# Optimization experiments

Measured on AMD Instinct MI355X. Metric: run time of the kernel, lower is better.

## Reference

```python
import jax, jax.numpy as jnp
import numpy as np

N = 50000      # nodes
E = 800000     # edges (avg degree 16)
G = 128        # graphs in batch
IN = 128       # in_channels
H = 128        # hidden_dim
C = 10         # num_classes


def setup_inputs() -> dict:
    key = jax.random.key(0)
    ks = jax.random.split(key, 8)
    x = jax.random.normal(ks[0], (N, IN), dtype=jnp.float32)
    edge_index = jax.random.randint(ks[1], (2, E), 0, N)
    edge_attr = jax.random.uniform(ks[2], (E,), dtype=jnp.float32)
    batch = jnp.sort(jax.random.randint(ks[3], (N,), 0, G))
    def glorot(k, fan_in, fan_out):
        return jax.random.normal(k, (fan_in, fan_out), dtype=jnp.float32) / np.float32(np.sqrt(fan_in))
    return {
        "x": x,
        "edge_index": edge_index,
        "edge_attr": edge_attr,
        "batch": batch,
        "W1": glorot(ks[4], IN, H), "b1": jnp.zeros((H,), jnp.float32),
        "W2": glorot(ks[5], H, H), "b2": jnp.zeros((H,), jnp.float32),
        "W3": glorot(ks[6], H, C), "b3": jnp.zeros((C,), jnp.float32),
    }


def gcn_conv(x, src, dst, ew, W, b, n):
    # symmetric GCN normalization (self-loops already appended, weight 1)
    deg = jax.ops.segment_sum(ew, dst, num_segments=n)            # [N]
    dinv = jnp.where(deg > 0, jax.lax.rsqrt(deg), 0.0)
    norm = dinv[src] * ew * dinv[dst]                             # [E+N]
    h = x @ W                                                     # [N, out]
    agg = jax.ops.segment_sum(h[src] * norm[:, None], dst, num_segments=n)
    return agg + b


def reference(x, edge_index, edge_attr, batch, W1, b1, W2, b2, W3, b3):
    n = x.shape[0]
    loop = jnp.arange(n)
    src = jnp.concatenate([edge_index[0], loop])
    dst = jnp.concatenate([edge_index[1], loop])
    ew = jnp.concatenate([edge_attr, jnp.ones((n,), edge_attr.dtype)])
    h = jax.nn.relu(gcn_conv(x, src, dst, ew, W1, b1, n))   # dropout is identity in eval
    h = jax.nn.relu(gcn_conv(h, src, dst, ew, W2, b2, n))
    h = gcn_conv(h, src, dst, ew, W3, b3, n)                 # [N, C]
    # global mean pool over graphs
    sums = jax.ops.segment_sum(h, batch, num_segments=G)     # [G, C]
    cnt = jax.ops.segment_sum(jnp.ones((n,), h.dtype), batch, num_segments=G)
    pooled = sums / jnp.maximum(cnt, 1.0)[:, None]
    return jax.nn.log_softmax(pooled, axis=1)
```

## Files before the change

### kernel.cpp

```cpp
#include <hip/hip_runtime.h>

#define NN 50000
#define NE 800000
#define NG 128
#define DIM 128
#define CO 10
#define CAP 64
#define NPB 2048
#define GEMB 782

typedef unsigned short ushort;
typedef unsigned int uint;
typedef __attribute__((ext_vector_type(8))) short short8;
typedef __attribute__((ext_vector_type(4))) float floatx4;

static __device__ __forceinline__ ushort f2bf(float f) {
    uint u = __float_as_uint(f);
    uint r = (u + 0x7FFF + ((u >> 16) & 1)) >> 16;
    return (ushort)r;
}
#define EWS (1.0f / 65535.0f)

__global__ void k_prep(const float* __restrict__ W1, const float* __restrict__ W2,
                       ushort* __restrict__ wt1, ushort* __restrict__ wt2,
                       int* __restrict__ cnt) {
    int i = blockIdx.x * 256 + threadIdx.x;
    if (i < 16384) {
        wt1[(i & 127) * 128 + (i >> 7)] = f2bf(W1[i]);
    } else if (i < 32768) {
        int j = i - 16384;
        wt2[(j & 127) * 128 + (j >> 7)] = f2bf(W2[j]);
    } else if (i < 32768 + NN) {
        cnt[i - 32768] = 0;
    }
}

__global__ void k_ell(const int* __restrict__ src, const int* __restrict__ dst,
                      const float* __restrict__ ew, int* __restrict__ cnt,
                      uint* __restrict__ ell) {
    int e = blockIdx.x * blockDim.x + threadIdx.x;
    if (e >= NE) return;
    int d = dst[e], s = src[e];
    int slot = atomicAdd(&cnt[d], 1);
    if (slot < CAP) {
        uint w16 = (uint)__float2uint_rn(ew[e] * 65535.0f);
        ell[(size_t)d * CAP + slot] = (w16 << 16) | (uint)s;
    }
}

static __device__ __forceinline__ void gemm_tile(const void* Ain, int abf,
                                                 const ushort* Wt,
                                                 const float* dglob, const float* dlds,
                                                 ushort* C, int M, int r0, int lane) {
    int quad = lane >> 4;
    int mcol = lane & 15;
    int arow = r0 + mcol;
    if (arow >= M) arow = M - 1;
    floatx4 acc[8];
#pragma unroll
    for (int t = 0; t < 8; t++) acc[t] = (floatx4){0.0f, 0.0f, 0.0f, 0.0f};
    const ushort* Ab = (const ushort*)Ain;
    const float*  Af = (const float*)Ain;
#pragma unroll
    for (int kk = 0; kk < 4; kk++) {
        int koff = kk * 32 + quad * 8;
        short8 a;
        if (abf) {
            a = *(const short8*)&Ab[(size_t)arow * 128 + koff];
        } else {
            const float* ap = &Af[(size_t)arow * 128 + koff];
            float4 x0 = *(const float4*)ap;
            float4 x1 = *(const float4*)(ap + 4);
            union { short8 v; ushort u[8]; } ua;
            ua.u[0] = f2bf(x0.x); ua.u[1] = f2bf(x0.y); ua.u[2] = f2bf(x0.z); ua.u[3] = f2bf(x0.w);
            ua.u[4] = f2bf(x1.x); ua.u[5] = f2bf(x1.y); ua.u[6] = f2bf(x1.z); ua.u[7] = f2bf(x1.w);
            a = ua.v;
        }
#pragma unroll
        for (int t = 0; t < 8; t++) {
            short8 b = *(const short8*)&Wt[(size_t)(t * 16 + mcol) * 128 + koff];
            acc[t] = __builtin_amdgcn_mfma_f32_16x16x32_bf16(a, b, acc[t], 0, 0, 0);
        }
    }
#pragma unroll
    for (int reg = 0; reg < 4; reg++) {
        int row = r0 + quad * 4 + reg;
        if (row < M) {
            float di = dglob ? dglob[row] : (dlds ? dlds[quad * 4 + reg] : 1.0f);
            ushort* cp = &C[(size_t)row * 128];
#pragma unroll
            for (int t = 0; t < 8; t++) cp[t * 16 + mcol] = f2bf(di * acc[t][reg]);
        }
    }
}

__global__ __launch_bounds__(256) void k_gemm1(const float* __restrict__ x,
                                               const ushort* __restrict__ wt1,
                                               const int* __restrict__ cnt,
                                               const uint* __restrict__ ell,
                                               float* __restrict__ dinv,
                                               ushort* __restrict__ hb) {
    __shared__ float sdinv[4][16];
    int wv = threadIdx.x >> 6;
    int lane = threadIdx.x & 63;
    int r0 = blockIdx.x * 64 + wv * 16;
#pragma unroll 4
    for (int r = 0; r < 16; r++) {
        int row = r0 + r;
        if (row < NN) {
            int n = cnt[row];
            float w = (lane < n) ? (float)(ell[(size_t)row * CAP + lane] >> 16) * EWS : 0.0f;
#pragma unroll
            for (int off = 32; off; off >>= 1) w += __shfl_down(w, off);
            if (lane == 0) {
                float dv = rsqrtf(1.0f + w);
                dinv[row] = dv;
                sdinv[wv][r] = dv;
            }
        }
    }
    gemm_tile(x, 0, wt1, nullptr, &sdinv[wv][0], hb, NN, r0, lane);
}

__global__ __launch_bounds__(256) void k_gemm2(const ushort* __restrict__ A,
                                               const ushort* __restrict__ wt2,
                                               const float* __restrict__ dinv,
                                               ushort* __restrict__ C) {
    int wv = threadIdx.x >> 6;
    int lane = threadIdx.x & 63;
    gemm_tile(A, 1, wt2, dinv, nullptr, C, NN, blockIdx.x * 64 + wv * 16, lane);
}

__global__ __launch_bounds__(256) void k_gather1(const int* __restrict__ cnt,
                                                 const uint* __restrict__ ell,
                                                 const float* __restrict__ dinv,
                                                 const ushort* __restrict__ h,
                                                 const float* __restrict__ b,
                                                 ushort* __restrict__ outp) {
    int node = blockIdx.x * 4 + (threadIdx.x >> 6);
    int lane = threadIdx.x & 63;
    if (node >= NN) return;
    int n = cnt[node];
    float di = dinv[node];
    uint rec = ell[(size_t)node * CAP + lane];
    int ce = (int)(rec & 0xffffu);
    float we = (float)(rec >> 16) * EWS;
    uint hp = *(const uint*)&h[(size_t)node * 128 + lane * 2];
    float ax = __uint_as_float(hp << 16);
    float ay = __uint_as_float(hp & 0xffff0000u);
    int j = 0;
    for (; j + 3 < n; j += 4) {
        int s0 = __shfl(ce, j + 0), s1 = __shfl(ce, j + 1);
        int s2 = __shfl(ce, j + 2), s3 = __shfl(ce, j + 3);
        float w0 = __shfl(we, j + 0), w1 = __shfl(we, j + 1);
        float w2 = __shfl(we, j + 2), w3 = __shfl(we, j + 3);
        uint p0 = *(const uint*)&h[(size_t)s0 * 128 + lane * 2];
        uint p1 = *(const uint*)&h[(size_t)s1 * 128 + lane * 2];
        uint p2 = *(const uint*)&h[(size_t)s2 * 128 + lane * 2];
        uint p3 = *(const uint*)&h[(size_t)s3 * 128 + lane * 2];
        ax += w0 * __uint_as_float(p0 << 16) + w1 * __uint_as_float(p1 << 16)
            + w2 * __uint_as_float(p2 << 16) + w3 * __uint_as_float(p3 << 16);
        ay += w0 * __uint_as_float(p0 & 0xffff0000u) + w1 * __uint_as_float(p1 & 0xffff0000u)
            + w2 * __uint_as_float(p2 & 0xffff0000u) + w3 * __uint_as_float(p3 & 0xffff0000u);
    }
    for (; j < n; j++) {
        int s0 = __shfl(ce, j);
        float w0 = __shfl(we, j);
        uint p0 = *(const uint*)&h[(size_t)s0 * 128 + lane * 2];
        ax += w0 * __uint_as_float(p0 << 16);
        ay += w0 * __uint_as_float(p0 & 0xffff0000u);
    }
    ax = fmaxf(di * ax + b[lane * 2 + 0], 0.0f);
    ay = fmaxf(di * ay + b[lane * 2 + 1], 0.0f);
    uint o = ((uint)f2bf(ay) << 16) | (uint)f2bf(ax);
    *(uint*)&outp[(size_t)node * 128 + lane * 2] = o;
}

__global__ __launch_bounds__(256) void k_gather2z(const int* __restrict__ cnt,
                                                  const uint* __restrict__ ell,
                                                  const float* __restrict__ dinv,
                                                  const ushort* __restrict__ h,
                                                  const float* __restrict__ b,
                                                  const float* __restrict__ W3,
                                                  float* __restrict__ z) {
    int lane = threadIdx.x & 63;
    int gwave = blockIdx.x * 4 + (threadIdx.x >> 6);
    float w3a[10], w3b[10];
    const float* wrow = &W3[lane * 20];
#pragma unroll
    for (int f = 0; f < 10; f++) { w3a[f] = wrow[f]; w3b[f] = wrow[10 + f]; }
    float bx = b[lane * 2 + 0], by = b[lane * 2 + 1];

    for (int node = gwave; node < NN; node += 12500) {
        int n = cnt[node];
        float di = dinv[node];
        uint rec = ell[(size_t)node * CAP + lane];
        int ce = (int)(rec & 0xffffu);
        float we = (float)(rec >> 16) * EWS;
        uint hp = *(const uint*)&h[(size_t)node * 128 + lane * 2];
        float ax = __uint_as_float(hp << 16);
        float ay = __uint_as_float(hp & 0xffff0000u);
        int j = 0;
        for (; j + 3 < n; j += 4) {
            int s0 = __shfl(ce, j + 0), s1 = __shfl(ce, j + 1);
            int s2 = __shfl(ce, j + 2), s3 = __shfl(ce, j + 3);
            float w0 = __shfl(we, j + 0), w1 = __shfl(we, j + 1);
            float w2 = __shfl(we, j + 2), w3 = __shfl(we, j + 3);
            uint p0 = *(const uint*)&h[(size_t)s0 * 128 + lane * 2];
            uint p1 = *(const uint*)&h[(size_t)s1 * 128 + lane * 2];
            uint p2 = *(const uint*)&h[(size_t)s2 * 128 + lane * 2];
            uint p3 = *(const uint*)&h[(size_t)s3 * 128 + lane * 2];
            ax += w0 * __uint_as_float(p0 << 16) + w1 * __uint_as_float(p1 << 16)
                + w2 * __uint_as_float(p2 << 16) + w3 * __uint_as_float(p3 << 16);
            ay += w0 * __uint_as_float(p0 & 0xffff0000u) + w1 * __uint_as_float(p1 & 0xffff0000u)
                + w2 * __uint_as_float(p2 & 0xffff0000u) + w3 * __uint_as_float(p3 & 0xffff0000u);
        }
        for (; j < n; j++) {
            int s0 = __shfl(ce, j);
            float w0 = __shfl(we, j);
            uint p0 = *(const uint*)&h[(size_t)s0 * 128 + lane * 2];
            ax += w0 * __uint_as_float(p0 << 16);
            ay += w0 * __uint_as_float(p0 & 0xffff0000u);
        }
        ax = fmaxf(di * ax + bx, 0.0f);
        ay = fmaxf(di * ay + by, 0.0f);
        float p[10];
#pragma unroll
        for (int f = 0; f < 10; f++) p[f] = ax * w3a[f] + ay * w3b[f];
#pragma unroll
        for (int off = 32; off; off >>= 1) {
#pragma unroll
            for (int f = 0; f < 10; f++) p[f] += __shfl_down(p[f], off);
        }
        if (lane == 0) {
            float* zp = &z[(size_t)node * 10];
#pragma unroll
            for (int f = 0; f < 10; f++) zp[f] = di * p[f];
        }
    }
}

__global__ __launch_bounds__(256) void k_pool_node(const int* __restrict__ cnt,
                                                   const uint* __restrict__ ell,
                                                   const float* __restrict__ dinv,
                                                   const float* __restrict__ z,
                                                   const int* __restrict__ batch,
                                                   float* __restrict__ partial) {
    __shared__ float ls[NG * CO + NG];
    for (int i = threadIdx.x; i < NG * CO + NG; i += 256) ls[i] = 0.0f;
    __syncthreads();
    int lane = threadIdx.x & 63;
    int gwave = blockIdx.x * 4 + (threadIdx.x >> 6);
    for (int node = gwave; node < NN; node += NPB * 4) {
        int n = cnt[node];
        float w = 0.0f; int s = 0;
        if (lane < n) {
            uint rec = ell[(size_t)node * CAP + lane];
            s = (int)(rec & 0xffffu);
            w = (float)(rec >> 16) * EWS;
        } else if (lane == n) {
            s = node;
            w = 1.0f;
        }
        const float* zp = &z[(size_t)s * 10];
        float v[10];
#pragma unroll
        for (int f = 0; f < 10; f++) v[f] = w * zp[f];
#pragma unroll
        for (int off = 32; off; off >>= 1) {
#pragma unroll
            for (int f = 0; f < 10; f++) v[f] += __shfl_down(v[f], off);
        }
        if (lane == 0) {
            int g = batch[node];
            float di = dinv[node];
            float* lp = &ls[g * 10];
#pragma unroll
            for (int f = 0; f < 10; f++) atomicAdd(&lp[f], di * v[f]);
            atomicAdd(&ls[NG * CO + g], 1.0f);
        }
    }
    __syncthreads();
    float* pb = &partial[(size_t)blockIdx.x * (NG * CO + NG)];
    for (int i = threadIdx.x; i < NG * CO + NG; i += 256) pb[i] = ls[i];
}

__global__ __launch_bounds__(256) void k_pool_final(const float* __restrict__ partial,
                                                    const float* __restrict__ b3,
                                                    float* __restrict__ out) {
    __shared__ float red[4][11];
    int g = blockIdx.x;
    int t = threadIdx.x;
    int lane = t & 63, wv = t >> 6;
    float v[10]; float c = 0.0f;
#pragma unroll
    for (int f = 0; f < 10; f++) v[f] = 0.0f;
    for (int b = t; b < NPB; b += 256) {
        const float* pb = &partial[(size_t)b * (NG * CO + NG)];
#pragma unroll
        for (int f = 0; f < 10; f++) v[f] += pb[g * 10 + f];
        c += pb[NG * CO + g];
    }
#pragma unroll
    for (int off = 32; off; off >>= 1) {
#pragma unroll
        for (int f = 0; f < 10; f++) v[f] += __shfl_down(v[f], off);
        c += __shfl_down(c, off);
    }
    if (lane == 0) {
#pragma unroll
        for (int f = 0; f < 10; f++) red[wv][f] = v[f];
        red[wv][10] = c;
    }
    __syncthreads();
    if (t == 0) {
        float p[10], m = -1e30f;
        float cc = red[0][10] + red[1][10] + red[2][10] + red[3][10];
        cc = fmaxf(cc, 1.0f);
#pragma unroll
        for (int f = 0; f < 10; f++) {
            p[f] = (red[0][f] + red[1][f] + red[2][f] + red[3][f]) / cc + b3[f];
            m = fmaxf(m, p[f]);
        }
        float ssum = 0.0f;
#pragma unroll
        for (int f = 0; f < 10; f++) ssum += __expf(p[f] - m);
        float lse = m + __logf(ssum);
#pragma unroll
        for (int f = 0; f < 10; f++) out[g * 10 + f] = p[f] - lse;
    }
}

extern "C" void kernel_launch(void* const* d_in, const int* in_sizes, int n_in,
                              void* d_out, int out_size, void* d_ws, size_t ws_size,
                              hipStream_t stream) {
    const float* x     = (const float*)d_in[0];
    const int*   ei    = (const int*)d_in[1];
    const float* ea    = (const float*)d_in[2];
    const int*   batch = (const int*)d_in[3];
    const float* W1    = (const float*)d_in[4];
    const float* b1    = (const float*)d_in[5];
    const float* W2    = (const float*)d_in[6];
    const float* b2    = (const float*)d_in[7];
    const float* W3    = (const float*)d_in[8];
    const float* b3    = (const float*)d_in[9];
    float* out = (float*)d_out;
    float* ws  = (float*)d_ws;

    const int* esrc = ei;
    const int* edst = ei + NE;

    ushort* hb      = (ushort*)ws;
    ushort* gb      = (ushort*)(ws + 3200000);
    float*  z       = ws + 6400000;
    float*  dinv    = ws + 6900000;
    int*    cnt     = (int*)(ws + 6950000);
    uint*   ell     = (uint*)(ws + 7000000);
    ushort* wt1     = (ushort*)(ws + 10200000);
    ushort* wt2     = (ushort*)(ws + 10210000);
    float*  partial = (float*)hb;

    k_prep<<<330, 256, 0, stream>>>(W1, W2, wt1, wt2, cnt);
    k_ell<<<(NE + 255) / 256, 256, 0, stream>>>(esrc, edst, ea, cnt, ell);
    k_gemm1<<<GEMB, 256, 0, stream>>>(x, wt1, cnt, ell, dinv, hb);
    k_gather1<<<(NN + 3) / 4, 256, 0, stream>>>(cnt, ell, dinv, hb, b1, gb);
    k_gemm2<<<GEMB, 256, 0, stream>>>(gb, wt2, dinv, hb);
    k_gather2z<<<3125, 256, 0, stream>>>(cnt, ell, dinv, hb, b2, W3, z);
    k_pool_node<<<NPB, 256, 0, stream>>>(cnt, ell, dinv, z, batch, partial);
    k_pool_final<<<NG, 256, 0, stream>>>(partial, b3, out);
}
```

Baseline: 325.0 us.

## Replace per-node atomic counters with sentinel-filled ELL rows and CAS slot insertion

Removes the per-destination counter array. Each edge is inserted with atomicCAS probing from a hashed slot into an ELL row pre-filled with a sentinel. Readers find the valid entries with a wave ballot and compact them with ds_permute, which gives both the count and the packed records. This avoids contended atomicAdd on counters, but it has to initialise the whole 50000x64 ELL array (12.8 MB) in the prep kernel and adds ballot/permute work to every gather.

```diff
diff --git a/kernel.cpp b/kernel.cpp
--- a/kernel.cpp
+++ b/kernel.cpp
@@ -8,7 +8,9 @@
 #define CAP 64
 #define NPB 2048
 #define GEMB 782
-
+#define SENT 0xFFFFFFFFu
+
+typedef unsigned long long ull;
 typedef unsigned short ushort;
 typedef unsigned int uint;
 typedef __attribute__((ext_vector_type(8))) short short8;
@@ -21,30 +23,55 @@
 }
 #define EWS (1.0f / 65535.0f)
 
+static __device__ __forceinline__ int row_load(const uint* __restrict__ ell,
+                                               int node, int lane,
+                                               int* ce, float* we) {
+    uint rec = ell[(size_t)node * CAP + lane];
+    bool valid = (rec != SENT);
+    ull mask = __ballot(valid);
+    int n = __popcll(mask);
+    ull below = (lane == 63) ? mask & ~(1ull << 63) : mask & ((1ull << lane) - 1ull);
+    int pos;
+    if (valid) {
+        pos = __popcll(below);
+    } else {
+        ull ibelow = ~mask & ((lane == 63) ? ~(1ull << 63) : ((1ull << lane) - 1ull));
+        pos = n + __popcll(ibelow);
+    }
+    uint crec = (uint)__builtin_amdgcn_ds_permute(pos << 2, (int)rec);
+    *ce = (int)(crec & 0xffffu);
+    *we = (float)(crec >> 16) * EWS;
+    return n;
+}
+
 __global__ void k_prep(const float* __restrict__ W1, const float* __restrict__ W2,
                        ushort* __restrict__ wt1, ushort* __restrict__ wt2,
-                       int* __restrict__ cnt) {
+                       uint* __restrict__ ell) {
     int i = blockIdx.x * 256 + threadIdx.x;
     if (i < 16384) {
         wt1[(i & 127) * 128 + (i >> 7)] = f2bf(W1[i]);
     } else if (i < 32768) {
         int j = i - 16384;
         wt2[(j & 127) * 128 + (j >> 7)] = f2bf(W2[j]);
-    } else if (i < 32768 + NN) {
-        cnt[i - 32768] = 0;
+    } else if (i < 32768 + NN * CAP) {
+        ell[i - 32768] = SENT;
     }
 }
 
 __global__ void k_ell(const int* __restrict__ src, const int* __restrict__ dst,
-                      const float* __restrict__ ew, int* __restrict__ cnt,
-                      uint* __restrict__ ell) {
+                      const float* __restrict__ ew, uint* __restrict__ ell) {
     int e = blockIdx.x * blockDim.x + threadIdx.x;
     if (e >= NE) return;
     int d = dst[e], s = src[e];
-    int slot = atomicAdd(&cnt[d], 1);
-    if (slot < CAP) {
-        uint w16 = (uint)__float2uint_rn(ew[e] * 65535.0f);
-        ell[(size_t)d * CAP + slot] = (w16 << 16) | (uint)s;
+    uint w16 = (uint)__float2uint_rn(ew[e] * 65535.0f);
+    uint rec = (w16 << 16) | (uint)s;
+    uint* row = &ell[(size_t)d * CAP];
+    uint h0 = (uint)e & 63u;
+#pragma unroll 1
+    for (int p = 0; p < CAP; p++) {
+        uint slot = (h0 + p) & 63u;
+        uint old = atomicCAS(&row[slot], SENT, rec);
+        if (old == SENT) break;
     }
 }
 
@@ -96,7 +123,6 @@
 
 __global__ __launch_bounds__(256) void k_gemm1(const float* __restrict__ x,
                                                const ushort* __restrict__ wt1,
-                                               const int* __restrict__ cnt,
                                                const uint* __restrict__ ell,
                                                float* __restrict__ dinv,
                                                ushort* __restrict__ hb) {
@@ -108,8 +134,8 @@
     for (int r = 0; r < 16; r++) {
         int row = r0 + r;
         if (row < NN) {
-            int n = cnt[row];
-            float w = (lane < n) ? (float)(ell[(size_t)row * CAP + lane] >> 16) * EWS : 0.0f;
+            uint rec = ell[(size_t)row * CAP + lane];
+            float w = (rec != SENT) ? (float)(rec >> 16) * EWS : 0.0f;
 #pragma unroll
             for (int off = 32; off; off >>= 1) w += __shfl_down(w, off);
             if (lane == 0) {
@@ -131,8 +157,7 @@
     gemm_tile(A, 1, wt2, dinv, nullptr, C, NN, blockIdx.x * 64 + wv * 16, lane);
 }
 
-__global__ __launch_bounds__(256) void k_gather1(const int* __restrict__ cnt,
-                                                 const uint* __restrict__ ell,
+__global__ __launch_bounds__(256) void k_gather1(const uint* __restrict__ ell,
                                                  const float* __restrict__ dinv,
                                                  const ushort* __restrict__ h,
                                                  const float* __restrict__ b,
@@ -140,11 +165,9 @@
     int node = blockIdx.x * 4 + (threadIdx.x >> 6);
     int lane = threadIdx.x & 63;
     if (node >= NN) return;
-    int n = cnt[node];
+    int ce; float we;
+    int n = row_load(ell, node, lane, &ce, &we);
     float di = dinv[node];
-    uint rec = ell[(size_t)node * CAP + lane];
-    int ce = (int)(rec & 0xffffu);
-    float we = (float)(rec >> 16) * EWS;
     uint hp = *(const uint*)&h[(size_t)node * 128 + lane * 2];
     float ax = __uint_as_float(hp << 16);
     float ay = __uint_as_float(hp & 0xffff0000u);
@@ -176,8 +199,7 @@
     *(uint*)&outp[(size_t)node * 128 + lane * 2] = o;
 }
 
-__global__ __launch_bounds__(256) void k_gather2z(const int* __restrict__ cnt,
-                                                  const uint* __restrict__ ell,
+__global__ __launch_bounds__(256) void k_gather2z(const uint* __restrict__ ell,
                                                   const float* __restrict__ dinv,
                                                   const ushort* __restrict__ h,
                                                   const float* __restrict__ b,
@@ -192,11 +214,9 @@
     float bx = b[lane * 2 + 0], by = b[lane * 2 + 1];
 
     for (int node = gwave; node < NN; node += 12500) {
-        int n = cnt[node];
+        int ce; float we;
+        int n = row_load(ell, node, lane, &ce, &we);
         float di = dinv[node];
-        uint rec = ell[(size_t)node * CAP + lane];
-        int ce = (int)(rec & 0xffffu);
-        float we = (float)(rec >> 16) * EWS;
         uint hp = *(const uint*)&h[(size_t)node * 128 + lane * 2];
         float ax = __uint_as_float(hp << 16);
         float ay = __uint_as_float(hp & 0xffff0000u);
@@ -240,8 +260,7 @@
     }
 }
 
-__global__ __launch_bounds__(256) void k_pool_node(const int* __restrict__ cnt,
-                                                   const uint* __restrict__ ell,
+__global__ __launch_bounds__(256) void k_pool_node(const uint* __restrict__ ell,
                                                    const float* __restrict__ dinv,
                                                    const float* __restrict__ z,
                                                    const int* __restrict__ batch,
@@ -252,12 +271,12 @@
     int lane = threadIdx.x & 63;
     int gwave = blockIdx.x * 4 + (threadIdx.x >> 6);
     for (int node = gwave; node < NN; node += NPB * 4) {
-        int n = cnt[node];
+        int ce; float we;
+        int n = row_load(ell, node, lane, &ce, &we);
         float w = 0.0f; int s = 0;
         if (lane < n) {
-            uint rec = ell[(size_t)node * CAP + lane];
-            s = (int)(rec & 0xffffu);
-            w = (float)(rec >> 16) * EWS;
+            s = ce;
+            w = we;
         } else if (lane == n) {
             s = node;
             w = 1.0f;
@@ -354,18 +373,17 @@
     ushort* gb      = (ushort*)(ws + 3200000);
     float*  z       = ws + 6400000;
     float*  dinv    = ws + 6900000;
-    int*    cnt     = (int*)(ws + 6950000);
     uint*   ell     = (uint*)(ws + 7000000);
     ushort* wt1     = (ushort*)(ws + 10200000);
     ushort* wt2     = (ushort*)(ws + 10210000);
     float*  partial = (float*)hb;
 
-    k_prep<<<330, 256, 0, stream>>>(W1, W2, wt1, wt2, cnt);
-    k_ell<<<(NE + 255) / 256, 256, 0, stream>>>(esrc, edst, ea, cnt, ell);
-    k_gemm1<<<GEMB, 256, 0, stream>>>(x, wt1, cnt, ell, dinv, hb);
-    k_gather1<<<(NN + 3) / 4, 256, 0, stream>>>(cnt, ell, dinv, hb, b1, gb);
+    k_prep<<<(32768 + NN * CAP + 255) / 256, 256, 0, stream>>>(W1, W2, wt1, wt2, ell);
+    k_ell<<<(NE + 255) / 256, 256, 0, stream>>>(esrc, edst, ea, ell);
+    k_gemm1<<<GEMB, 256, 0, stream>>>(x, wt1, ell, dinv, hb);
+    k_gather1<<<(NN + 3) / 4, 256, 0, stream>>>(ell, dinv, hb, b1, gb);
     k_gemm2<<<GEMB, 256, 0, stream>>>(gb, wt2, dinv, hb);
-    k_gather2z<<<3125, 256, 0, stream>>>(cnt, ell, dinv, hb, b2, W3, z);
-    k_pool_node<<<NPB, 256, 0, stream>>>(cnt, ell, dinv, z, batch, partial);
+    k_gather2z<<<3125, 256, 0, stream>>>(ell, dinv, hb, b2, W3, z);
+    k_pool_node<<<NPB, 256, 0, stream>>>(ell, dinv, z, batch, partial);
     k_pool_final<<<NG, 256, 0, stream>>>(partial, b3, out);
 }
```

Measured after the change: 326.8 us. No clear change (+0.6%).
